# Optimization experiments

Hardware: AMD Instinct MI355X
Metric: run time of the kernel (lower is better)

Reference implementation:

```python
import jax, jax.numpy as jnp
import numpy as np

DT = 0.002   # solver step used for drive indexing
B = 2097152  # batched independent circuits (trailing axis of y)
T = 50000    # external drive time steps
NP = 59      # number of clamped scalar parameters


def setup_inputs() -> dict:
    key = jax.random.key(0)
    k1, k2, k3 = jax.random.split(key, 3)
    params = jax.random.uniform(k1, (NP,), jnp.float32, 0.5, 10.0)
    bounds_lo = jnp.full((NP,), 0.01, dtype=jnp.float32)
    bounds_hi = jnp.full((NP,), 100.0, dtype=jnp.float32)
    t = jnp.float32(12.345)
    y = jax.random.normal(k2, (12, B), jnp.float32) * 5.0
    external_drive = jax.random.normal(k3, (T, 6), jnp.float32)
    return {"params": params, "bounds_lo": bounds_lo, "bounds_hi": bounds_hi,
            "t": t, "y": y, "external_drive": external_drive}


def _S(v, e0, v0, r):
    # sigmoidal firing-rate function
    return 2.0 * e0 / (1.0 + jnp.exp(r * (v0 - v)))


def reference(params, bounds_lo, bounds_hi, t, y, external_drive):
    p = jnp.clip(params, bounds_lo, bounds_hi)
    (A_p23_p23, A_p23_p5, A_p23_st, A_p23_PV, A_p23_SST, A_p23_VIP, a_p23, e0_p23, v0_p23, r_p23,
     A_p5_p5, A_p5_st, A_p5_PV, A_p5_SST, a_p5, e0_p5, v0_p5, r_p5,
     A_st_p23, A_st_p5, A_st_st, A_st_PV, A_st_SST, a_st, e0_st, v0_st, r_st,
     B_PV_p23, B_PV_p5, B_PV_st, B_PV_PV, B_PV_SST, B_PV_VIP, b_PV, e0_PV, v0_PV, r_PV,
     B_SST_p23, B_SST_p5, B_SST_PV, B_SST_SST, B_SST_VIP, b_SST, e0_SST, v0_SST, r_SST,
     B_VIP_PV, B_VIP_SST, B_VIP_VIP, b_VIP, e0_VIP, v0_VIP, r_VIP,
     N_p23, N_p5, N_st, N_PV, N_SST, N_VIP) = p

    P23, P5, St, PV, SST, VIP, dP23, dP5, dSt, dPV, dSST, dVIP = y  # each [B]

    F_P23 = _S(P23, e0_p23, v0_p23, r_p23)
    F_P5  = _S(P5,  e0_p5,  v0_p5,  r_p5)
    F_St  = _S(St,  e0_st,  v0_st,  r_st)
    F_PV  = _S(PV,  e0_PV,  v0_PV,  r_PV)
    F_SST = _S(SST, e0_SST, v0_SST, r_SST)
    F_VIP = _S(VIP, e0_VIP, v0_VIP, r_VIP)

    n_t = external_drive.shape[0]
    t_idx = jnp.clip(t / DT, 0.0, n_t - 1).astype(jnp.int32)
    drive = jax.lax.dynamic_index_in_dim(external_drive, t_idx, axis=0, keepdims=False)  # [6]
    cc_p23, th_p5, th_st, th_PV, nm_SST, cc_VIP = drive[0], drive[1], drive[2], drive[3], drive[4], drive[5]

    dy6 = (cc_p23 + A_st_p23 * a_st * F_St * (N_st / N_p23)
           + A_p23_p23 * a_p23 * F_P23
           - B_PV_p23 * b_PV * F_PV * (N_PV / N_p23)
           - B_SST_p23 * b_SST * F_SST * (N_SST / N_p23)
           - 2.0 * a_p23 * dP23 - a_p23 ** 2 * P23)
    dy7 = (th_p5 + A_st_p5 * a_st * F_St * (N_st / N_p5)
           + A_p23_p5 * a_p23 * F_P23 * (N_p23 / N_p5)
           + A_p5_p5 * a_p5 * F_P5
           - B_PV_p5 * b_PV * F_PV * (N_PV / N_p5)
           - B_SST_p5 * b_SST * F_SST * (N_SST / N_p5)
           - 2.0 * a_p5 * dP5 - a_p5 ** 2 * P5)
    dy8 = (th_st + A_p23_st * a_p23 * F_P23 * (N_p23 / N_st)
           + A_p5_st * a_p5 * F_P5 * (N_p5 / N_st)
           - B_PV_st * b_PV * F_PV * (N_PV / N_st)
           - 2.0 * a_st * dSt - a_st ** 2 * St)
    dy9 = (th_PV + A_p23_PV * a_p23 * F_P23 * (N_p23 / N_PV)
           + A_p5_PV * a_p5 * F_P5 * (N_p5 / N_PV)
           + A_st_PV * a_st * F_St * (N_st / N_PV)
           - B_PV_PV * b_PV * F_PV
           - B_SST_PV * b_SST * F_SST * (N_SST / N_PV)
           - B_VIP_PV * b_VIP * F_VIP * (N_VIP / N_PV)
           - 2.0 * b_PV * dPV - b_PV ** 2 * PV)
    dy10 = (nm_SST + A_p23_SST * a_p23 * F_P23 * (N_p23 / N_SST)
            + A_p5_SST * a_p5 * F_P5 * (N_p5 / N_SST)
            + A_st_SST * a_st * F_St * (N_st / N_SST)
            - B_PV_SST * b_PV * F_PV * (N_PV / N_SST)
            - B_SST_SST * b_SST * F_SST
            - B_VIP_SST * b_VIP * F_VIP * (N_VIP / N_SST)
            - 2.0 * b_SST * dSST - b_SST ** 2 * SST)
    dy11 = (cc_VIP + A_p23_VIP * a_p23 * F_P23 * (N_p23 / N_VIP)
            - B_PV_VIP * b_PV * F_PV * (N_PV / N_VIP)
            - B_SST_VIP * b_SST * F_SST * (N_SST / N_VIP)
            - B_VIP_VIP * b_VIP * F_VIP
            - 2.0 * b_VIP * dVIP - b_VIP ** 2 * VIP)

    return jnp.stack([dP23, dP5, dSt, dPV, dSST, dVIP, dy6, dy7, dy8, dy9, dy10, dy11])
```

## Files before the change

### kernel.cpp

```cpp
#include <hip/hip_runtime.h>
#include <math.h>


typedef float v4f __attribute__((ext_vector_type(4)));

__global__ void setup_kernel(
    const float* __restrict__ params,
    const float* __restrict__ blo,
    const float* __restrict__ bhi,
    const float* __restrict__ tptr,
    const float* __restrict__ drive,
    float* __restrict__ sc_out,
    int tsteps)
{
    __shared__ float p[59];
    const int tid = threadIdx.x;
    if (tid < 59) {
        float v = params[tid];
        p[tid] = fminf(fmaxf(v, blo[tid]), bhi[tid]);
    }
    __syncthreads();
    if (tid != 0) return;

    float A_p23_p23=p[0], A_p23_p5=p[1], A_p23_st=p[2], A_p23_PV=p[3],
          A_p23_SST=p[4], A_p23_VIP=p[5], a_p23=p[6], e0_p23=p[7],
          v0_p23=p[8], r_p23=p[9];
    float A_p5_p5=p[10], A_p5_st=p[11], A_p5_PV=p[12], A_p5_SST=p[13],
          a_p5=p[14], e0_p5=p[15], v0_p5=p[16], r_p5=p[17];
    float A_st_p23=p[18], A_st_p5=p[19], A_st_PV=p[21],
          A_st_SST=p[22], a_st=p[23], e0_st=p[24], v0_st=p[25], r_st=p[26];
    float B_PV_p23=p[27], B_PV_p5=p[28], B_PV_st=p[29], B_PV_PV=p[30],
          B_PV_SST=p[31], B_PV_VIP=p[32], b_PV=p[33], e0_PV=p[34],
          v0_PV=p[35], r_PV=p[36];
    float B_SST_p23=p[37], B_SST_p5=p[38], B_SST_PV=p[39], B_SST_SST=p[40],
          B_SST_VIP=p[41], b_SST=p[42], e0_SST=p[43], v0_SST=p[44], r_SST=p[45];
    float B_VIP_PV=p[46], B_VIP_SST=p[47], B_VIP_VIP=p[48], b_VIP=p[49],
          e0_VIP=p[50], v0_VIP=p[51], r_VIP=p[52];
    float N_p23=p[53], N_p5=p[54], N_st=p[55], N_PV=p[56], N_SST=p[57], N_VIP=p[58];

    const float rr[6] = {r_p23, r_p5, r_st, r_PV, r_SST, r_VIP};
    const float vv[6] = {v0_p23, v0_p5, v0_st, v0_PV, v0_SST, v0_VIP};
    const float ee[6] = {e0_p23, e0_p5, e0_st, e0_PV, e0_SST, e0_VIP};
    const float gg[6] = {a_p23, a_p5, a_st, b_PV, b_SST, b_VIP};
    for (int k = 0; k < 6; ++k) {
        sc_out[k]      = rr[k];
        sc_out[6 + k]  = rr[k] * vv[k];
        sc_out[12 + k] = 2.0f * ee[k];
        sc_out[18 + k] = 2.0f * gg[k];
        sc_out[24 + k] = gg[k] * gg[k];
    }

    float t = *tptr;
    float fi = fminf(fmaxf(t / 0.002f, 0.0f), (float)(tsteps - 1));
    int ti = (int)fi;
    for (int k = 0; k < 6; ++k) sc_out[30 + k] = drive[(size_t)ti * 6 + k];

    float M[36];
    for (int i = 0; i < 36; ++i) M[i] = 0.0f;
    M[0*6+0] =  A_p23_p23 * a_p23;
    M[0*6+2] =  A_st_p23  * a_st  * (N_st  / N_p23);
    M[0*6+3] = -B_PV_p23  * b_PV  * (N_PV  / N_p23);
    M[0*6+4] = -B_SST_p23 * b_SST * (N_SST / N_p23);

    M[1*6+0] =  A_p23_p5  * a_p23 * (N_p23 / N_p5);
    M[1*6+1] =  A_p5_p5   * a_p5;
    M[1*6+2] =  A_st_p5   * a_st  * (N_st  / N_p5);
    M[1*6+3] = -B_PV_p5   * b_PV  * (N_PV  / N_p5);
    M[1*6+4] = -B_SST_p5  * b_SST * (N_SST / N_p5);

    M[2*6+0] =  A_p23_st  * a_p23 * (N_p23 / N_st);
    M[2*6+1] =  A_p5_st   * a_p5  * (N_p5  / N_st);
    M[2*6+3] = -B_PV_st   * b_PV  * (N_PV  / N_st);

    M[3*6+0] =  A_p23_PV  * a_p23 * (N_p23 / N_PV);
    M[3*6+1] =  A_p5_PV   * a_p5  * (N_p5  / N_PV);
    M[3*6+2] =  A_st_PV   * a_st  * (N_st  / N_PV);
    M[3*6+3] = -B_PV_PV   * b_PV;
    M[3*6+4] = -B_SST_PV  * b_SST * (N_SST / N_PV);
    M[3*6+5] = -B_VIP_PV  * b_VIP * (N_VIP / N_PV);

    M[4*6+0] =  A_p23_SST * a_p23 * (N_p23 / N_SST);
    M[4*6+1] =  A_p5_SST  * a_p5  * (N_p5  / N_SST);
    M[4*6+2] =  A_st_SST  * a_st  * (N_st  / N_SST);
    M[4*6+3] = -B_PV_SST  * b_PV  * (N_PV  / N_SST);
    M[4*6+4] = -B_SST_SST * b_SST;
    M[4*6+5] = -B_VIP_SST * b_VIP * (N_VIP / N_SST);

    M[5*6+0] =  A_p23_VIP * a_p23 * (N_p23 / N_VIP);
    M[5*6+3] = -B_PV_VIP  * b_PV  * (N_PV  / N_VIP);
    M[5*6+4] = -B_SST_VIP * b_SST * (N_SST / N_VIP);
    M[5*6+5] = -B_VIP_VIP * b_VIP;

    for (int i = 0; i < 36; ++i) sc_out[36 + i] = M[i];
}

__global__ __launch_bounds__(256) void cc_kernel(
    const float* __restrict__ y,
    const float* __restrict__ scg,
    float* __restrict__ out,
    int n)
{
    __shared__ float sc[72];
    if (threadIdx.x < 72) sc[threadIdx.x] = scg[threadIdx.x];
    __syncthreads();

    const size_t i4 = ((size_t)blockIdx.x * blockDim.x + threadIdx.x) * 4;
    if (i4 >= (size_t)n) return;

    v4f v[12];
#pragma unroll
    for (int r = 0; r < 12; ++r)
        v[r] = *(const v4f*)(y + (size_t)r * n + i4);

#pragma unroll
    for (int r = 0; r < 6; ++r)
        *(v4f*)(out + (size_t)r * n + i4) = v[6 + r];

    float F[6][4];
#pragma unroll
    for (int k = 0; k < 6; ++k) {
        const float rk  = sc[k];
        const float rv0 = sc[6 + k];
        const float e2  = sc[12 + k];
#pragma unroll
        for (int j = 0; j < 4; ++j)
            F[k][j] = e2 / (1.0f + __expf(rv0 - rk * v[k][j]));
    }

#pragma unroll
    for (int i = 0; i < 6; ++i) {
        const float dr  = sc[30 + i];
        const float tg  = sc[18 + i];
        const float gsq = sc[24 + i];
        v4f o;
#pragma unroll
        for (int j = 0; j < 4; ++j) {
            float acc = dr;
#pragma unroll
            for (int k = 0; k < 6; ++k)
                acc = fmaf(sc[36 + i * 6 + k], F[k][j], acc);
            acc = fmaf(-tg, v[6 + i][j], acc);
            acc = fmaf(-gsq, v[i][j], acc);
            o[j] = acc;
        }
        *(v4f*)(out + (size_t)(6 + i) * n + i4) = o;
    }
}

extern "C" void kernel_launch(void* const* d_in, const int* in_sizes, int n_in,
                              void* d_out, int out_size, void* d_ws, size_t ws_size,
                              hipStream_t stream) {
    const float* params = (const float*)d_in[0];
    const float* blo    = (const float*)d_in[1];
    const float* bhi    = (const float*)d_in[2];
    const float* tptr   = (const float*)d_in[3];
    const float* y      = (const float*)d_in[4];
    const float* drive  = (const float*)d_in[5];
    float* out = (float*)d_out;
    float* sc  = (float*)d_ws;

    const int n      = in_sizes[4] / 12;
    const int tsteps = in_sizes[5] / 6;

    setup_kernel<<<1, 64, 0, stream>>>(params, blo, bhi, tptr, drive, sc, tsteps);

    const int threads = 256;
    const int elems_per_block = threads * 4;
    const int blocks = (n + elems_per_block - 1) / elems_per_block;

    cc_kernel<<<blocks, threads, 0, stream>>>(y, sc, out, n);
}
```

Baseline: 41.47 us.

## Fuse parameter setup into main kernel and process two vec4 chunks per thread

```diff
diff --git a/kernel.cpp b/kernel.cpp
--- a/kernel.cpp
+++ b/kernel.cpp
@@ -4,118 +4,25 @@
 
 typedef float v4f __attribute__((ext_vector_type(4)));
 
-__global__ void setup_kernel(
-    const float* __restrict__ params,
-    const float* __restrict__ blo,
-    const float* __restrict__ bhi,
-    const float* __restrict__ tptr,
-    const float* __restrict__ drive,
-    float* __restrict__ sc_out,
-    int tsteps)
+__device__ const unsigned char CIDX[36] = {
+    0, 255,  18,  27,  37, 255,
+    1,  10,  19,  28,  38, 255,
+    2,  11, 255,  29, 255, 255,
+    3,  12,  21,  30,  39,  46,
+    4,  13,  22,  31,  40,  47,
+    5, 255, 255,  32,  41,  48
+};
+__device__ const unsigned char GIDX[6] = {6, 14, 23, 33, 42, 49};
+__device__ const unsigned char NIDX[6] = {53, 54, 55, 56, 57, 58};
+__device__ const unsigned char RIDX[6] = {9, 17, 26, 36, 45, 52};
+__device__ const unsigned char VIDX[6] = {8, 16, 25, 35, 44, 51};
+__device__ const unsigned char EIDX[6] = {7, 15, 24, 34, 43, 50};
+
+__device__ __forceinline__ void compute6(const v4f* __restrict__ v,
+                                         const float* __restrict__ sc,
+                                         float* __restrict__ out,
+                                         size_t base, size_t n)
 {
-    __shared__ float p[59];
-    const int tid = threadIdx.x;
-    if (tid < 59) {
-        float v = params[tid];
-        p[tid] = fminf(fmaxf(v, blo[tid]), bhi[tid]);
-    }
-    __syncthreads();
-    if (tid != 0) return;
-
-    float A_p23_p23=p[0], A_p23_p5=p[1], A_p23_st=p[2], A_p23_PV=p[3],
-          A_p23_SST=p[4], A_p23_VIP=p[5], a_p23=p[6], e0_p23=p[7],
-          v0_p23=p[8], r_p23=p[9];
-    float A_p5_p5=p[10], A_p5_st=p[11], A_p5_PV=p[12], A_p5_SST=p[13],
-          a_p5=p[14], e0_p5=p[15], v0_p5=p[16], r_p5=p[17];
-    float A_st_p23=p[18], A_st_p5=p[19], A_st_PV=p[21],
-          A_st_SST=p[22], a_st=p[23], e0_st=p[24], v0_st=p[25], r_st=p[26];
-    float B_PV_p23=p[27], B_PV_p5=p[28], B_PV_st=p[29], B_PV_PV=p[30],
-          B_PV_SST=p[31], B_PV_VIP=p[32], b_PV=p[33], e0_PV=p[34],
-          v0_PV=p[35], r_PV=p[36];
-    float B_SST_p23=p[37], B_SST_p5=p[38], B_SST_PV=p[39], B_SST_SST=p[40],
-          B_SST_VIP=p[41], b_SST=p[42], e0_SST=p[43], v0_SST=p[44], r_SST=p[45];
-    float B_VIP_PV=p[46], B_VIP_SST=p[47], B_VIP_VIP=p[48], b_VIP=p[49],
-          e0_VIP=p[50], v0_VIP=p[51], r_VIP=p[52];
-    float N_p23=p[53], N_p5=p[54], N_st=p[55], N_PV=p[56], N_SST=p[57], N_VIP=p[58];
-
-    const float rr[6] = {r_p23, r_p5, r_st, r_PV, r_SST, r_VIP};
-    const float vv[6] = {v0_p23, v0_p5, v0_st, v0_PV, v0_SST, v0_VIP};
-    const float ee[6] = {e0_p23, e0_p5, e0_st, e0_PV, e0_SST, e0_VIP};
-    const float gg[6] = {a_p23, a_p5, a_st, b_PV, b_SST, b_VIP};
-    for (int k = 0; k < 6; ++k) {
-        sc_out[k]      = rr[k];
-        sc_out[6 + k]  = rr[k] * vv[k];
-        sc_out[12 + k] = 2.0f * ee[k];
-        sc_out[18 + k] = 2.0f * gg[k];
-        sc_out[24 + k] = gg[k] * gg[k];
-    }
-
-    float t = *tptr;
-    float fi = fminf(fmaxf(t / 0.002f, 0.0f), (float)(tsteps - 1));
-    int ti = (int)fi;
-    for (int k = 0; k < 6; ++k) sc_out[30 + k] = drive[(size_t)ti * 6 + k];
-
-    float M[36];
-    for (int i = 0; i < 36; ++i) M[i] = 0.0f;
-    M[0*6+0] =  A_p23_p23 * a_p23;
-    M[0*6+2] =  A_st_p23  * a_st  * (N_st  / N_p23);
-    M[0*6+3] = -B_PV_p23  * b_PV  * (N_PV  / N_p23);
-    M[0*6+4] = -B_SST_p23 * b_SST * (N_SST / N_p23);
-
-    M[1*6+0] =  A_p23_p5  * a_p23 * (N_p23 / N_p5);
-    M[1*6+1] =  A_p5_p5   * a_p5;
-    M[1*6+2] =  A_st_p5   * a_st  * (N_st  / N_p5);
-    M[1*6+3] = -B_PV_p5   * b_PV  * (N_PV  / N_p5);
-    M[1*6+4] = -B_SST_p5  * b_SST * (N_SST / N_p5);
-
-    M[2*6+0] =  A_p23_st  * a_p23 * (N_p23 / N_st);
-    M[2*6+1] =  A_p5_st   * a_p5  * (N_p5  / N_st);
-    M[2*6+3] = -B_PV_st   * b_PV  * (N_PV  / N_st);
-
-    M[3*6+0] =  A_p23_PV  * a_p23 * (N_p23 / N_PV);
-    M[3*6+1] =  A_p5_PV   * a_p5  * (N_p5  / N_PV);
-    M[3*6+2] =  A_st_PV   * a_st  * (N_st  / N_PV);
-    M[3*6+3] = -B_PV_PV   * b_PV;
-    M[3*6+4] = -B_SST_PV  * b_SST * (N_SST / N_PV);
-    M[3*6+5] = -B_VIP_PV  * b_VIP * (N_VIP / N_PV);
-
-    M[4*6+0] =  A_p23_SST * a_p23 * (N_p23 / N_SST);
-    M[4*6+1] =  A_p5_SST  * a_p5  * (N_p5  / N_SST);
-    M[4*6+2] =  A_st_SST  * a_st  * (N_st  / N_SST);
-    M[4*6+3] = -B_PV_SST  * b_PV  * (N_PV  / N_SST);
-    M[4*6+4] = -B_SST_SST * b_SST;
-    M[4*6+5] = -B_VIP_SST * b_VIP * (N_VIP / N_SST);
-
-    M[5*6+0] =  A_p23_VIP * a_p23 * (N_p23 / N_VIP);
-    M[5*6+3] = -B_PV_VIP  * b_PV  * (N_PV  / N_VIP);
-    M[5*6+4] = -B_SST_VIP * b_SST * (N_SST / N_VIP);
-    M[5*6+5] = -B_VIP_VIP * b_VIP;
-
-    for (int i = 0; i < 36; ++i) sc_out[36 + i] = M[i];
-}
-
-__global__ __launch_bounds__(256) void cc_kernel(
-    const float* __restrict__ y,
-    const float* __restrict__ scg,
-    float* __restrict__ out,
-    int n)
-{
-    __shared__ float sc[72];
-    if (threadIdx.x < 72) sc[threadIdx.x] = scg[threadIdx.x];
-    __syncthreads();
-
-    const size_t i4 = ((size_t)blockIdx.x * blockDim.x + threadIdx.x) * 4;
-    if (i4 >= (size_t)n) return;
-
-    v4f v[12];
-#pragma unroll
-    for (int r = 0; r < 12; ++r)
-        v[r] = *(const v4f*)(y + (size_t)r * n + i4);
-
-#pragma unroll
-    for (int r = 0; r < 6; ++r)
-        *(v4f*)(out + (size_t)r * n + i4) = v[6 + r];
-
     float F[6][4];
 #pragma unroll
     for (int k = 0; k < 6; ++k) {
@@ -126,7 +33,6 @@
         for (int j = 0; j < 4; ++j)
             F[k][j] = e2 / (1.0f + __expf(rv0 - rk * v[k][j]));
     }
-
 #pragma unroll
     for (int i = 0; i < 6; ++i) {
         const float dr  = sc[30 + i];
@@ -143,8 +49,90 @@
             acc = fmaf(-gsq, v[i][j], acc);
             o[j] = acc;
         }
-        *(v4f*)(out + (size_t)(6 + i) * n + i4) = o;
+        *(v4f*)(out + (size_t)(6 + i) * n + base) = o;
     }
+}
+
+__global__ __launch_bounds__(256) void cc_kernel(
+    const float* __restrict__ params,
+    const float* __restrict__ blo,
+    const float* __restrict__ bhi,
+    const float* __restrict__ tptr,
+    const float* __restrict__ y,
+    const float* __restrict__ drive,
+    float* __restrict__ out,
+    int n, int tsteps)
+{
+    __shared__ float p[59];
+    __shared__ float sc[72];
+    const int tid = threadIdx.x;
+
+    if (tid < 59)
+        p[tid] = fminf(fmaxf(params[tid], blo[tid]), bhi[tid]);
+    __syncthreads();
+
+    if (tid < 72) {
+        float v;
+        if (tid < 6) {
+            v = p[RIDX[tid]];
+        } else if (tid < 12) {
+            const int k = tid - 6;  v = p[RIDX[k]] * p[VIDX[k]];
+        } else if (tid < 18) {
+            const int k = tid - 12; v = 2.0f * p[EIDX[k]];
+        } else if (tid < 24) {
+            const int k = tid - 18; v = 2.0f * p[GIDX[k]];
+        } else if (tid < 30) {
+            const int k = tid - 24; const float g = p[GIDX[k]]; v = g * g;
+        } else if (tid < 36) {
+            const int k = tid - 30;
+            const float t = *tptr;
+            const float fi = fminf(fmaxf(t / 0.002f, 0.0f), (float)(tsteps - 1));
+            const int ti = (int)fi;
+            v = drive[(size_t)ti * 6 + k];
+        } else {
+            const int l = tid - 36;
+            const int i = l / 6, j = l - i * 6;
+            const int c = CIDX[l];
+            if (c == 255) {
+                v = 0.0f;
+            } else {
+                float m = p[c] * p[GIDX[j]];
+                if (i != j) m = m * (p[NIDX[j]] / p[NIDX[i]]);
+                if (j >= 3) m = -m;
+                v = m;
+            }
+        }
+        sc[tid] = v;
+    }
+    __syncthreads();
+
+    const size_t n_ = (size_t)n;
+    const size_t b0 = (size_t)blockIdx.x * 2048 + (size_t)tid * 4;
+    const size_t b1 = b0 + 1024;
+    if (b0 >= n_) return;
+    const bool do1 = (b1 + 3 < n_);
+
+    v4f va[12], vb[12];
+#pragma unroll
+    for (int r = 0; r < 12; ++r)
+        va[r] = *(const v4f*)(y + (size_t)r * n_ + b0);
+    if (do1) {
+#pragma unroll
+        for (int r = 0; r < 12; ++r)
+            vb[r] = *(const v4f*)(y + (size_t)r * n_ + b1);
+    }
+
+#pragma unroll
+    for (int r = 0; r < 6; ++r)
+        *(v4f*)(out + (size_t)r * n_ + b0) = va[6 + r];
+    if (do1) {
+#pragma unroll
+        for (int r = 0; r < 6; ++r)
+            *(v4f*)(out + (size_t)r * n_ + b1) = vb[6 + r];
+    }
+
+    compute6(va, sc, out, b0, n_);
+    if (do1) compute6(vb, sc, out, b1, n_);
 }
 
 extern "C" void kernel_launch(void* const* d_in, const int* in_sizes, int n_in,
@@ -157,16 +145,14 @@
     const float* y      = (const float*)d_in[4];
     const float* drive  = (const float*)d_in[5];
     float* out = (float*)d_out;
-    float* sc  = (float*)d_ws;
 
     const int n      = in_sizes[4] / 12;
     const int tsteps = in_sizes[5] / 6;
 
-    setup_kernel<<<1, 64, 0, stream>>>(params, blo, bhi, tptr, drive, sc, tsteps);
-
     const int threads = 256;
-    const int elems_per_block = threads * 4;
+    const int elems_per_block = threads * 8;
     const int blocks = (n + elems_per_block - 1) / elems_per_block;
 
-    cc_kernel<<<blocks, threads, 0, stream>>>(y, sc, out, n);
+    cc_kernel<<<blocks, threads, 0, stream>>>(params, blo, bhi, tptr, y, drive,
+                                              out, n, tsteps);
 }
```

Result: slower. 43.03 us (+3.8%).
